# Optimization experiments

Hardware: AMD Instinct MI355X
Metric: run time of the kernel (lower is better)

## Reference

```python
import jax, jax.numpy as jnp
import numpy as np
import math

DIM = 384; HEADS = 12; HD = 32; L_REL = 4; L_STD = 12; MLP_H = 4 * DIM
B = 8; N = 256
N_REL = 1
TIME_SCALE = 30000.0 / 500 * 0.3
SCALE = HD ** -0.5
NEG = -1e9  # finite stand-in for -inf padding mask (identical softmax result, safe grads)


def _ln(x, g, b):
    m = x.mean(-1, keepdims=True)
    v = ((x - m) ** 2).mean(-1, keepdims=True)
    return (x - m) / jnp.sqrt(v + 1e-5) * g + b


def _sin_emb(x, dim):
    half = dim // 2
    freq = jnp.exp(jnp.arange(half, dtype=x.dtype) * (-math.log(10000.0) / half))
    e = x[..., None] * freq
    return jnp.concatenate([jnp.sin(e), jnp.cos(e)], -1)


def _rel_bias(x0, w1d, b1d, wp, bp):
    pos = x0[..., :3]
    t = x0[..., 3:4]
    dpos = pos[:, :, None] - pos[:, None, :]                 # [B,N,N,3]
    dt = t[:, :, None] - t[:, None, :] * TIME_SCALE          # [B,N,N,1] (scale on 2nd term, as in torch)
    dpos2 = dpos ** 2
    dt2 = dt ** 2
    ds2 = dpos2.sum(-1) - dt2[..., 0]
    d = jnp.sign(ds2) * jnp.sqrt(jnp.abs(ds2))
    f = jnp.concatenate([dpos, dt, dpos2, dt2], -1)          # [B,N,N,8]
    d = d + (f @ w1d.T + b1d)[..., 0]
    emb = _sin_emb(1024.0 * jnp.clip(d, -4.0, 4.0), HD)      # [B,N,N,HD]
    return emb @ wp.T + bp


def _mask_bias(mask):
    mn = jnp.minimum(mask[:, None, :], mask[:, :, None])
    mx = jnp.maximum(mask[:, None, :], mask[:, :, None])
    return jnp.where(mx < 0, 0.0, mn)                        # [B,N,N]


def _attn(xq, xkv, wq, wk, wv, wo, bo, rel, mbias):
    Bq, Nq, _ = xq.shape
    q = (xq @ wq.T).reshape(Bq, Nq, HEADS, HD).transpose(0, 2, 1, 3) * SCALE
    k = (xkv @ wk.T).reshape(Bq, Nq, HEADS, HD).transpose(0, 2, 1, 3)
    v = (xkv @ wv.T).reshape(Bq, Nq, HEADS, HD).transpose(0, 2, 1, 3)
    a = jnp.einsum('bhic,bhjc->bhij', q, k)
    if rel is not None:
        a = a + jnp.einsum('bhic,bijc->bhij', q, rel)
    if mbias is not None:
        a = a + mbias[:, None]
    a = jax.nn.softmax(a, axis=-1)
    o = jnp.einsum('bhij,bhjc->bihc', a, v)
    if rel is not None:
        o = o + jnp.einsum('bhij,bijc->bihc', a, rel)
    return o.reshape(Bq, Nq, HEADS * HD) @ wo.T + bo


def _mlp(x, w1, b1, w2, b2):
    return jax.nn.gelu(x @ w1.T + b1, approximate=False) @ w2.T + b2


def setup_inputs() -> dict:
    key = jax.random.key(0)
    ks = iter(jax.random.split(key, 64))
    f = lambda shape: jax.random.normal(next(ks), shape, jnp.float32) * 0.02
    inp = {}
    inp['x'] = jax.random.normal(next(ks), (B, N, DIM), jnp.float32)
    inp['x0'] = jax.random.normal(next(ks), (B, N, 4), jnp.float32)
    lengths = jax.random.randint(next(ks), (B,), N // 2, N + 1)
    inp['mask'] = jnp.where(jnp.arange(N)[None, :] < lengths[:, None], 0.0, NEG).astype(jnp.float32)
    inp['rp_w1d'] = f((1, 8)); inp['rp_b1d'] = jnp.zeros((1,), jnp.float32)
    inp['rp_wp'] = f((HD, HD)); inp['rp_bp'] = jnp.zeros((HD,), jnp.float32)
    for p, L in (('sw', L_REL), ('bl', L_STD)):
        inp[p + '_ln1_g'] = jnp.ones((L, DIM), jnp.float32); inp[p + '_ln1_b'] = jnp.zeros((L, DIM), jnp.float32)
        inp[p + '_ln2_g'] = jnp.ones((L, DIM), jnp.float32); inp[p + '_ln2_b'] = jnp.zeros((L, DIM), jnp.float32)
        inp[p + '_wq'] = f((L, DIM, DIM)); inp[p + '_wk'] = f((L, DIM, DIM)); inp[p + '_wv'] = f((L, DIM, DIM))
        inp[p + '_wo'] = f((L, DIM, DIM)); inp[p + '_bo'] = jnp.zeros((L, DIM), jnp.float32)
        inp[p + '_w1'] = f((L, MLP_H, DIM)); inp[p + '_b1'] = jnp.zeros((L, MLP_H), jnp.float32)
        inp[p + '_w2'] = f((L, DIM, MLP_H)); inp[p + '_b2'] = jnp.zeros((L, DIM), jnp.float32)
    inp['bl_g1'] = jnp.ones((L_STD, DIM), jnp.float32)   # init_values=1
    inp['bl_g2'] = jnp.ones((L_STD, DIM), jnp.float32)
    inp['cls_w'] = f((DIM,))
    inp['out_w'] = f((3, DIM)); inp['out_b'] = jnp.zeros((3,), jnp.float32)
    return inp


def reference(x, x0, mask, rp_w1d, rp_b1d, rp_wp, rp_bp,
              sw_ln1_g, sw_ln1_b, sw_ln2_g, sw_ln2_b, sw_wq, sw_wk, sw_wv, sw_wo, sw_bo,
              sw_w1, sw_b1, sw_w2, sw_b2,
              bl_ln1_g, bl_ln1_b, bl_ln2_g, bl_ln2_b, bl_wq, bl_wk, bl_wv, bl_wo, bl_bo,
              bl_w1, bl_b1, bl_w2, bl_b2, bl_g1, bl_g2, cls_w, out_w, out_b):
    rel = _rel_bias(x0, rp_w1d, rp_b1d, rp_wp, rp_bp)
    mbias = _mask_bias(mask)
    for i in range(L_REL):
        r = rel if i < N_REL else None
        xn = _ln(x, sw_ln1_g[i], sw_ln1_b[i])
        x = x + _attn(xn, xn, sw_wq[i], sw_wk[i], sw_wv[i], sw_wo[i], sw_bo[i], r, mbias)
        x = x + _mlp(_ln(x, sw_ln2_g[i], sw_ln2_b[i]), sw_w1[i], sw_b1[i], sw_w2[i], sw_b2[i])
    # prepend cls token; it is always valid
    cls = jnp.broadcast_to(cls_w[None, None, :], (x.shape[0], 1, DIM))
    x = jnp.concatenate([cls, x], axis=1)
    mask2 = jnp.concatenate([jnp.zeros((x.shape[0], 1), mask.dtype), mask], axis=1)
    mbias2 = _mask_bias(mask2)
    for i in range(L_STD):
        xn = _ln(x, bl_ln1_g[i], bl_ln1_b[i])
        x = x + bl_g1[i] * _attn(xn, xn, bl_wq[i], bl_wk[i], bl_wv[i], bl_wo[i], bl_bo[i], None, mbias2)
        x = x + bl_g2[i] * _mlp(_ln(x, bl_ln2_g[i], bl_ln2_b[i]), bl_w1[i], bl_b1[i], bl_w2[i], bl_b2[i])
    return x[:, 0] @ out_w.T + out_b   # [B, 3]
```

## Files before the change

kernel.cpp:

```cpp
#include <hip/hip_runtime.h>
#include <hip/hip_bf16.h>
#include <math.h>

#define DIM 384
#define HEADS 12
#define HD 32
#define MLP_H 1536
#define BATCH 8
#define N1 256
#define N2 257
#define QP 1152
#define SCALE 0.17677669529663687f
#define TIME_SCALE 18.0f

typedef __attribute__((ext_vector_type(8))) short frag8;
typedef __attribute__((ext_vector_type(4))) float f32x4;

__device__ inline short f2bf(float x) {
    __hip_bfloat16 h = __float2bfloat16(x);
    short s;
    __builtin_memcpy(&s, &h, 2);
    return s;
}
__device__ inline float bf2f(short s) {
    unsigned u = ((unsigned)(unsigned short)s) << 16;
    float f;
    __builtin_memcpy(&f, &u, 4);
    return f;
}

__global__ __launch_bounds__(256) void conv_kernel(
        const float* __restrict__ in, short* __restrict__ out, int n) {
    int i = (blockIdx.x * 256 + threadIdx.x) * 4;
    if (i >= n) return;
    float4 v = *(const float4*)(in + i);
    out[i]     = f2bf(v.x);
    out[i + 1] = f2bf(v.y);
    out[i + 2] = f2bf(v.z);
    out[i + 3] = f2bf(v.w);
}

__global__ __launch_bounds__(256) void conv_qkv_kernel(
        const float* __restrict__ wq, const float* __restrict__ wk,
        const float* __restrict__ wv, short* __restrict__ out, int L) {
    size_t idx = ((size_t)blockIdx.x * 256 + threadIdx.x) * 4;
    size_t total = (size_t)L * QP * DIM;
    if (idx >= total) return;
    size_t k = idx % DIM;
    size_t row = idx / DIM;
    size_t r = row % QP;
    size_t l = row / QP;
    int which = (int)(r / DIM);
    int rr = (int)(r % DIM);
    const float* src = ((which == 0) ? wq : (which == 1) ? wk : wv)
                     + (l * DIM + rr) * DIM + k;
    float4 v = *(const float4*)src;
    out[idx]     = f2bf(v.x);
    out[idx + 1] = f2bf(v.y);
    out[idx + 2] = f2bf(v.z);
    out[idx + 3] = f2bf(v.w);
}

__global__ __launch_bounds__(256) void rel_kernel(
        const float* __restrict__ x0, const float* __restrict__ w1d,
        const float* __restrict__ b1d, const float* __restrict__ wp,
        const float* __restrict__ bp, short* __restrict__ rel) {
    __shared__ float sw1[8];
    __shared__ float sb1s[1];
    __shared__ short scr[4][64][40];
    int tid = threadIdx.x;
    int w = tid >> 6, lane = tid & 63;
    int n = lane & 15, quad = lane >> 4;
    if (tid < 8) sw1[tid] = w1d[tid];
    if (tid == 0) sb1s[0] = b1d[0];

    frag8 wb0, wb1;
    #pragma unroll
    for (int e = 0; e < 8; e++) {
        wb0[e] = f2bf(wp[n * 32 + quad * 8 + e]);
        wb1[e] = f2bf(wp[(n + 16) * 32 + quad * 8 + e]);
    }
    float bp0 = bp[n], bp1 = bp[n + 16];
    __syncthreads();
    float sb1 = sb1s[0];

    int gbase = blockIdx.x * 256 + w * 64;
    int gid = gbase + lane;
    int j  = gid & (N1 - 1);
    int bi = gid >> 8;
    int i  = bi & (N1 - 1);
    int b  = bi >> 8;

    const float* pi = x0 + (size_t)(b * N1 + i) * 4;
    const float* pj = x0 + (size_t)(b * N1 + j) * 4;
    float dx = pi[0] - pj[0], dy = pi[1] - pj[1], dz = pi[2] - pj[2];
    float dt = pi[3] - pj[3] * TIME_SCALE;
    float dx2 = dx * dx, dy2 = dy * dy, dz2 = dz * dz, dt2 = dt * dt;
    float ds2 = dx2 + dy2 + dz2 - dt2;
    float d = copysignf(sqrtf(fabsf(ds2)), ds2);
    d += dx * sw1[0] + dy * sw1[1] + dz * sw1[2] + dt * sw1[3]
       + dx2 * sw1[4] + dy2 * sw1[5] + dz2 * sw1[6] + dt2 * sw1[7] + sb1;
    d = fminf(fmaxf(d, -4.f), 4.f) * 1024.f;

    const float freq[16] = {
        1.0f, 0.56234132519f, 0.31622776602f, 0.17782794100f,
        0.1f, 0.056234132519f, 0.031622776602f, 0.017782794100f,
        0.01f, 0.0056234132519f, 0.0031622776602f, 0.0017782794100f,
        0.001f, 0.00056234132519f, 0.00031622776602f, 0.00017782794100f};
    #pragma unroll
    for (int k = 0; k < 16; k++) {
        float rev = d * freq[k] * 0.15915494309189535f;
        rev = rev - floorf(rev);
        float s = __builtin_amdgcn_sinf(rev);
        float c = __builtin_amdgcn_cosf(rev);
        scr[w][lane][k]      = f2bf(s);
        scr[w][lane][16 + k] = f2bf(c);
    }

    #pragma unroll
    for (int g16 = 0; g16 < 4; g16++) {
        frag8 ea = *(const frag8*)&scr[w][g16 * 16 + n][quad * 8];
        f32x4 z = {0.f, 0.f, 0.f, 0.f};
        f32x4 s0 = __builtin_amdgcn_mfma_f32_16x16x32_bf16(ea, wb0, z, 0, 0, 0);
        f32x4 s1 = __builtin_amdgcn_mfma_f32_16x16x32_bf16(ea, wb1, z, 0, 0, 0);
        #pragma unroll
        for (int r = 0; r < 4; r++) {
            scr[w][g16 * 16 + quad * 4 + r][n]      = f2bf(s0[r] + bp0);
            scr[w][g16 * 16 + quad * 4 + r][n + 16] = f2bf(s1[r] + bp1);
        }
    }

    short* dst = rel + (size_t)gbase * HD;
    #pragma unroll
    for (int s = 0; s < 4; s++) {
        frag8 v = *(const frag8*)&scr[w][s * 16 + (lane >> 2)][(lane & 3) * 8];
        *(frag8*)(dst + s * 512 + lane * 8) = v;
    }
}

__global__ __launch_bounds__(256) void rel_score_kernel(
        const short* __restrict__ qkv, const short* __restrict__ relb,
        short* __restrict__ rs) {
    int tid = threadIdx.x;
    int w = tid >> 6, lane = tid & 63;
    int n = lane & 15, quad = lane >> 4;
    int i = blockIdx.x * 4 + w;
    int b = blockIdx.y;

    const frag8 fz = {0, 0, 0, 0, 0, 0, 0, 0};
    frag8 qa = fz;
    if (n < HEADS)
        qa = *(const frag8*)(qkv + ((size_t)(b * N1) + i) * QP + n * HD + quad * 8);

    const short* relrow = relb + (((size_t)(b * N1) + i) * N1) * HD;
    const f32x4 z = {0.f, 0.f, 0.f, 0.f};

    #pragma unroll 4
    for (int jt = 0; jt < 16; jt++) {
        frag8 rb = *(const frag8*)(relrow + (size_t)(jt * 16 + n) * HD + quad * 8);
        f32x4 s = __builtin_amdgcn_mfma_f32_16x16x32_bf16(qa, rb, z, 0, 0, 0);
        #pragma unroll
        for (int r = 0; r < 4; r++) {
            int h = quad * 4 + r;
            if (h < HEADS)
                rs[((size_t)(b * HEADS + h) * N1 + i) * N1 + jt * 16 + n] =
                    f2bf(s[r] * SCALE);
        }
    }
}

__global__ __launch_bounds__(256) void rel_pv_kernel(
        const short* __restrict__ pglob, const short* __restrict__ relb,
        const float* __restrict__ omain, short* __restrict__ ob) {
    __shared__ short vt[4][2][2][64][8];
    int tid = threadIdx.x;
    int w = tid >> 6, lane = tid & 63;
    int n = lane & 15, quad = lane >> 4;
    int i = blockIdx.x * 4 + w;
    int b = blockIdx.y;
    size_t rowB = (size_t)(b * N1);

    const frag8 fz = {0, 0, 0, 0, 0, 0, 0, 0};
    f32x4 oa0 = {0.f, 0.f, 0.f, 0.f}, oa1 = {0.f, 0.f, 0.f, 0.f};
    const short* relrow = relb + ((rowB + i) * (size_t)N1) * HD;
    const short* prow = pglob + ((size_t)(b * HEADS + (n < HEADS ? n : 0)) * N1 + i) * N1;
    bool hval = (n < HEADS);

    int jr = lane & 31;
    int cb = (lane >> 5) * 16;

    #pragma unroll 2
    for (int kk = 0; kk < 8; kk++) {
        int par = kk & 1;
        const short* rr = relrow + (size_t)(kk * 32 + jr) * HD + cb;
        frag8 rv0 = *(const frag8*)rr;
        frag8 rv1 = *(const frag8*)(rr + 8);
        #pragma unroll
        for (int e = 0; e < 8; e++) {
            int c0 = cb + e, c1 = cb + 8 + e;
            vt[w][par][c0 >> 4][(jr >> 3) * 16 + (c0 & 15)][jr & 7] = rv0[e];
            vt[w][par][c1 >> 4][(jr >> 3) * 16 + (c1 & 15)][jr & 7] = rv1[e];
        }
        frag8 pa = fz;
        if (hval) pa = *(const frag8*)(prow + kk * 32 + quad * 8);
        frag8 b0 = *(const frag8*)&vt[w][par][0][lane][0];
        frag8 b1 = *(const frag8*)&vt[w][par][1][lane][0];
        oa0 = __builtin_amdgcn_mfma_f32_16x16x32_bf16(pa, b0, oa0, 0, 0, 0);
        oa1 = __builtin_amdgcn_mfma_f32_16x16x32_bf16(pa, b1, oa1, 0, 0, 0);
    }

    #pragma unroll
    for (int r = 0; r < 4; r++) {
        int h = quad * 4 + r;
        if (h < HEADS) {
            size_t o0 = (rowB + i) * DIM + h * HD + n;
            ob[o0]      = f2bf(omain[o0]      + oa0[r]);
            ob[o0 + 16] = f2bf(omain[o0 + 16] + oa1[r]);
        }
    }
}

__global__ __launch_bounds__(128) void ln_kernel(
        const float* __restrict__ x, const float* __restrict__ g,
        const float* __restrict__ b, short* __restrict__ y) {
    int r = blockIdx.x;
    int t = threadIdx.x;
    const float* xr = x + (size_t)r * DIM;
    float v0 = xr[t], v1 = xr[t + 128], v2 = xr[t + 256];
    __shared__ float redm[2], redv[2];
    float s = v0 + v1 + v2;
    for (int o = 32; o; o >>= 1) s += __shfl_down(s, o, 64);
    int lane = t & 63, wid = t >> 6;
    if (!lane) redm[wid] = s;
    __syncthreads();
    float mean = (redm[0] + redm[1]) * (1.f / DIM);
    float d0 = v0 - mean, d1 = v1 - mean, d2 = v2 - mean;
    float s2 = d0 * d0 + d1 * d1 + d2 * d2;
    for (int o = 32; o; o >>= 1) s2 += __shfl_down(s2, o, 64);
    if (!lane) redv[wid] = s2;
    __syncthreads();
    float var = (redv[0] + redv[1]) * (1.f / DIM);
    float rs = rsqrtf(var + 1e-5f);
    short* yr = y + (size_t)r * DIM;
    yr[t]       = f2bf(d0 * rs * g[t]       + b[t]);
    yr[t + 128] = f2bf(d1 * rs * g[t + 128] + b[t + 128]);
    yr[t + 256] = f2bf(d2 * rs * g[t + 256] + b[t + 256]);
}

__global__ __launch_bounds__(512) void gemm_bf16_kernel(
        const short* __restrict__ A, const short* __restrict__ W,
        const float* __restrict__ bias, const float* __restrict__ resid,
        const float* __restrict__ gvec, float* __restrict__ Cf,
        short* __restrict__ Cb, int M, int Np, int K, int mode) {
    __shared__ short As2[2][2][4][64][8];
    __shared__ short Bs2[2][2][4][64][8];
    int tid = threadIdx.x;
    int w = tid >> 6, lane = tid & 63;
    int nlo = lane & 15, quad = lane >> 4;
    int g = w >> 2, wl = w & 3;
    int wm = wl >> 1, wn = wl & 1;
    int n0 = blockIdx.x * 64, m0 = blockIdx.y * 64;

    f32x4 acc00 = {0.f, 0.f, 0.f, 0.f}, acc01 = {0.f, 0.f, 0.f, 0.f};
    f32x4 acc10 = {0.f, 0.f, 0.f, 0.f}, acc11 = {0.f, 0.f, 0.f, 0.f};

    int oct16 = tid & 15, rbase = tid >> 4;
    int kh_s = oct16 >> 3, oo = oct16 & 7, ks_s = oo >> 2, q_s = oo & 3;
    const frag8 fz = {0, 0, 0, 0, 0, 0, 0, 0};
    frag8 pa0 = fz, pa1 = fz, pb0, pb1;

    {
        int gm0 = m0 + rbase, gm1 = m0 + rbase + 32;
        if (gm0 < M) pa0 = *(const frag8*)(A + (size_t)gm0 * K + oct16 * 8);
        if (gm1 < M) pa1 = *(const frag8*)(A + (size_t)gm1 * K + oct16 * 8);
        pb0 = *(const frag8*)(W + (size_t)(n0 + rbase) * K + oct16 * 8);
        pb1 = *(const frag8*)(W + (size_t)(n0 + rbase + 32) * K + oct16 * 8);
    }

    for (int k0 = 0; k0 < K; k0 += 128) {
        *(frag8*)&As2[kh_s][ks_s][q_s][rbase][0]      = pa0;
        *(frag8*)&As2[kh_s][ks_s][q_s][rbase + 32][0] = pa1;
        *(frag8*)&Bs2[kh_s][ks_s][q_s][rbase][0]      = pb0;
        *(frag8*)&Bs2[kh_s][ks_s][q_s][rbase + 32][0] = pb1;
        __syncthreads();
        int kn = k0 + 128;
        if (kn < K) {
            int gm0 = m0 + rbase, gm1 = m0 + rbase + 32;
            pa0 = fz; pa1 = fz;
            if (gm0 < M) pa0 = *(const frag8*)(A + (size_t)gm0 * K + kn + oct16 * 8);
            if (gm1 < M) pa1 = *(const frag8*)(A + (size_t)gm1 * K + kn + oct16 * 8);
            pb0 = *(const frag8*)(W + (size_t)(n0 + rbase) * K + kn + oct16 * 8);
            pb1 = *(const frag8*)(W + (size_t)(n0 + rbase + 32) * K + kn + oct16 * 8);
        }
        #pragma unroll
        for (int ks = 0; ks < 2; ks++) {
            frag8 a0 = *(const frag8*)&As2[g][ks][quad][wm * 32 + nlo][0];
            frag8 a1 = *(const frag8*)&As2[g][ks][quad][wm * 32 + 16 + nlo][0];
            frag8 b0 = *(const frag8*)&Bs2[g][ks][quad][wn * 32 + nlo][0];
            frag8 b1 = *(const frag8*)&Bs2[g][ks][quad][wn * 32 + 16 + nlo][0];
            acc00 = __builtin_amdgcn_mfma_f32_16x16x32_bf16(a0, b0, acc00, 0, 0, 0);
            acc01 = __builtin_amdgcn_mfma_f32_16x16x32_bf16(a0, b1, acc01, 0, 0, 0);
            acc10 = __builtin_amdgcn_mfma_f32_16x16x32_bf16(a1, b0, acc10, 0, 0, 0);
            acc11 = __builtin_amdgcn_mfma_f32_16x16x32_bf16(a1, b1, acc11, 0, 0, 0);
        }
        __syncthreads();
    }

    f32x4* red4 = (f32x4*)&As2[0][0][0][0][0];
    int roff = wl * 64 + lane;
    if (g == 1) {
        red4[roff]       = acc00;
        red4[256 + roff] = acc01;
        red4[512 + roff] = acc10;
        red4[768 + roff] = acc11;
    }
    __syncthreads();
    if (g == 1) return;
    {
        f32x4 t0 = red4[roff], t1 = red4[256 + roff];
        f32x4 t2 = red4[512 + roff], t3 = red4[768 + roff];
        #pragma unroll
        for (int r = 0; r < 4; r++) {
            acc00[r] += t0[r]; acc01[r] += t1[r];
            acc10[r] += t2[r]; acc11[r] += t3[r];
        }
    }

    #pragma unroll
    for (int mi = 0; mi < 2; mi++) {
        #pragma unroll
        for (int nf = 0; nf < 2; nf++) {
            f32x4 av = (mi == 0) ? ((nf == 0) ? acc00 : acc01)
                                 : ((nf == 0) ? acc10 : acc11);
            int col = n0 + wn * 32 + nf * 16 + nlo;
            float bcol = (mode >= 1) ? bias[col] : 0.f;
            float gs = 1.f;
            if (mode == 2 && gvec) gs = gvec[col];
            #pragma unroll
            for (int r = 0; r < 4; r++) {
                int row = m0 + wm * 32 + mi * 16 + quad * 4 + r;
                if (row >= M) continue;
                float v = av[r] + bcol;
                if (mode == 1) v = 0.5f * v * (1.f + erff(v * 0.70710678118654752f));
                if (mode == 2) {
                    Cf[(size_t)row * Np + col] = resid[(size_t)row * Np + col] + gs * v;
                } else {
                    Cb[(size_t)row * Np + col] = f2bf(v);
                }
            }
        }
    }
}

__global__ __launch_bounds__(256) void attn_mfma_kernel(
        const short* __restrict__ qkv, const float* __restrict__ maskv,
        short* __restrict__ ob, int Nseq) {
    __shared__ short kf[18][64][8];
    __shared__ short vf[9][2][64][8];
    __shared__ short pbuf[4][2][16][40];
    __shared__ float ms[320];

    int tid = threadIdx.x;
    int w = tid >> 6, lane = tid & 63;
    int n = lane & 15, quad = lane >> 4;
    int qg = blockIdx.x, h = blockIdx.y, b = blockIdx.z;
    size_t rowB = (size_t)(b * Nseq);

    for (int j = tid; j < 320; j += 256)
        ms[j] = (j < Nseq) ? maskv[b * Nseq + j] : 0.f;

    {
        int c0 = (tid & 3) * 8;
        for (int j = tid >> 2; j < 288; j += 64) {
            frag8 kk = {0, 0, 0, 0, 0, 0, 0, 0};
            frag8 vv = {0, 0, 0, 0, 0, 0, 0, 0};
            if (j < Nseq) {
                const short* base = qkv + (rowB + j) * QP + h * HD + c0;
                kk = *(const frag8*)(base + 384);
                vv = *(const frag8*)(base + 768);
            }
            *(frag8*)&kf[j >> 4][(c0 >> 3) * 16 + (j & 15)][0] = kk;
            #pragma unroll
            for (int e = 0; e < 8; e++) {
                int c = c0 + e;
                vf[j >> 5][c >> 4][((j & 31) >> 3) * 16 + (c & 15)][j & 7] = vv[e];
            }
        }
    }

    int i0 = qg * 64 + w * 16;
    frag8 qa = {0, 0, 0, 0, 0, 0, 0, 0};
    {
        int i = i0 + n;
        if (i < Nseq) qa = *(const frag8*)(qkv + (rowB + i) * QP + h * HD + quad * 8);
    }
    __syncthreads();

    float msq[4];
    #pragma unroll
    for (int r = 0; r < 4; r++) msq[r] = ms[i0 + quad * 4 + r];

    float mrow[4], lsum[4];
    #pragma unroll
    for (int r = 0; r < 4; r++) { mrow[r] = -3.0e38f; lsum[r] = 0.f; }
    f32x4 oacc0 = {0.f, 0.f, 0.f, 0.f}, oacc1 = {0.f, 0.f, 0.f, 0.f};

    for (int jb = 0; jb < 9; jb++) {
        int par = jb & 1;
        frag8 kb0 = *(const frag8*)&kf[2 * jb][lane][0];
        frag8 kb1 = *(const frag8*)&kf[2 * jb + 1][lane][0];
        f32x4 z = {0.f, 0.f, 0.f, 0.f};
        f32x4 s0 = __builtin_amdgcn_mfma_f32_16x16x32_bf16(qa, kb0, z, 0, 0, 0);
        f32x4 s1 = __builtin_amdgcn_mfma_f32_16x16x32_bf16(qa, kb1, z, 0, 0, 0);

        int j0 = jb * 32 + n;
        int j1 = j0 + 16;
        float mj0 = ms[j0], mj1 = ms[j1];
        float pad0 = (j0 < Nseq) ? 0.f : -1e9f;
        float pad1 = (j1 < Nseq) ? 0.f : -1e9f;

        #pragma unroll
        for (int r = 0; r < 4; r++) {
            float mi = msq[r];
            float b0 = ((fmaxf(mi, mj0) < 0.f) ? 0.f : fminf(mi, mj0)) + pad0;
            float b1 = ((fmaxf(mi, mj1) < 0.f) ? 0.f : fminf(mi, mj1)) + pad1;
            float v0 = s0[r] * SCALE + b0;
            float v1 = s1[r] * SCALE + b1;
            float rm = fmaxf(v0, v1);
            rm = fmaxf(rm, __shfl_xor(rm, 1));
            rm = fmaxf(rm, __shfl_xor(rm, 2));
            rm = fmaxf(rm, __shfl_xor(rm, 4));
            rm = fmaxf(rm, __shfl_xor(rm, 8));
            float mn = fmaxf(mrow[r], rm);
            float alpha = __expf(mrow[r] - mn);
            mrow[r] = mn;
            float p0 = __expf(v0 - mn);
            float p1 = __expf(v1 - mn);
            float ps = p0 + p1;
            ps += __shfl_xor(ps, 1);
            ps += __shfl_xor(ps, 2);
            ps += __shfl_xor(ps, 4);
            ps += __shfl_xor(ps, 8);
            lsum[r] = lsum[r] * alpha + ps;
            oacc0[r] *= alpha;
            oacc1[r] *= alpha;
            pbuf[w][par][quad * 4 + r][n]      = f2bf(p0);
            pbuf[w][par][quad * 4 + r][n + 16] = f2bf(p1);
        }
        frag8 pa = *(const frag8*)&pbuf[w][par][n][quad * 8];
        frag8 vb0 = *(const frag8*)&vf[jb][0][lane][0];
        frag8 vb1 = *(const frag8*)&vf[jb][1][lane][0];
        oacc0 = __builtin_amdgcn_mfma_f32_16x16x32_bf16(pa, vb0, oacc0, 0, 0, 0);
        oacc1 = __builtin_amdgcn_mfma_f32_16x16x32_bf16(pa, vb1, oacc1, 0, 0, 0);
    }

    #pragma unroll
    for (int r = 0; r < 4; r++) {
        int i = i0 + quad * 4 + r;
        if (i < Nseq) {
            float invl = 1.f / lsum[r];
            ob[(rowB + i) * DIM + h * HD + n]      = f2bf(oacc0[r] * invl);
            ob[(rowB + i) * DIM + h * HD + 16 + n] = f2bf(oacc1[r] * invl);
        }
    }
}

__global__ __launch_bounds__(128) void attn_rel_mfma_kernel(
        const short* __restrict__ qkv, short* __restrict__ rs,
        const float* __restrict__ maskv, float* __restrict__ omain) {
    const int Nseq = N1;
    __shared__ short kf[16][64][8];
    __shared__ short vf[8][2][64][8];
    __shared__ short pbuf[2][2][16][40];
    __shared__ float ms[256];

    int tid = threadIdx.x;
    int w = tid >> 6, lane = tid & 63;
    int n = lane & 15, quad = lane >> 4;
    int qg = blockIdx.x, h = blockIdx.y, b = blockIdx.z;
    size_t rowB = (size_t)(b * Nseq);

    for (int jj = tid; jj < 256; jj += 128) ms[jj] = maskv[b * Nseq + jj];

    {
        int c0 = (tid & 3) * 8;
        for (int j = tid >> 2; j < 256; j += 32) {
            const short* base = qkv + (rowB + j) * QP + h * HD + c0;
            frag8 kk = *(const frag8*)(base + 384);
            frag8 vv = *(const frag8*)(base + 768);
            *(frag8*)&kf[j >> 4][(c0 >> 3) * 16 + (j & 15)][0] = kk;
            #pragma unroll
            for (int e = 0; e < 8; e++) {
                int c = c0 + e;
                vf[j >> 5][c >> 4][((j & 31) >> 3) * 16 + (c & 15)][j & 7] = vv[e];
            }
        }
    }

    int i0 = qg * 32 + w * 16;
    frag8 qa = *(const frag8*)(qkv + (rowB + i0 + n) * QP + h * HD + quad * 8);
    __syncthreads();

    float msq[4];
    short* rsp[4];
    #pragma unroll
    for (int r = 0; r < 4; r++) {
        msq[r] = ms[i0 + quad * 4 + r];
        rsp[r] = rs + ((size_t)(b * HEADS + h) * N1 + (i0 + quad * 4 + r)) * N1;
    }

    float sv0[32], sv1[32];
    float rmax[4];
    #pragma unroll
    for (int r = 0; r < 4; r++) rmax[r] = -3.0e38f;

    #pragma unroll
    for (int jb = 0; jb < 8; jb++) {
        frag8 kb0 = *(const frag8*)&kf[2 * jb][lane][0];
        frag8 kb1 = *(const frag8*)&kf[2 * jb + 1][lane][0];
        f32x4 z = {0.f, 0.f, 0.f, 0.f};
        f32x4 s0 = __builtin_amdgcn_mfma_f32_16x16x32_bf16(qa, kb0, z, 0, 0, 0);
        f32x4 s1 = __builtin_amdgcn_mfma_f32_16x16x32_bf16(qa, kb1, z, 0, 0, 0);
        int j0 = jb * 32 + n;
        int j1 = j0 + 16;
        float mj0 = ms[j0], mj1 = ms[j1];
        #pragma unroll
        for (int r = 0; r < 4; r++) {
            float d0 = bf2f(rsp[r][j0]);
            float d1 = bf2f(rsp[r][j1]);
            float mi = msq[r];
            float b0 = (fmaxf(mi, mj0) < 0.f) ? 0.f : fminf(mi, mj0);
            float b1 = (fmaxf(mi, mj1) < 0.f) ? 0.f : fminf(mi, mj1);
            float v0 = s0[r] * SCALE + d0 + b0;
            float v1 = s1[r] * SCALE + d1 + b1;
            sv0[jb * 4 + r] = v0;
            sv1[jb * 4 + r] = v1;
            rmax[r] = fmaxf(rmax[r], fmaxf(v0, v1));
        }
    }
    #pragma unroll
    for (int r = 0; r < 4; r++) {
        float rm = rmax[r];
        rm = fmaxf(rm, __shfl_xor(rm, 1));
        rm = fmaxf(rm, __shfl_xor(rm, 2));
        rm = fmaxf(rm, __shfl_xor(rm, 4));
        rm = fmaxf(rm, __shfl_xor(rm, 8));
        rmax[r] = rm;
    }

    float lsum[4] = {0.f, 0.f, 0.f, 0.f};
    #pragma unroll
    for (int jb = 0; jb < 8; jb++) {
        #pragma unroll
        for (int r = 0; r < 4; r++) {
            float p0 = __expf(sv0[jb * 4 + r] - rmax[r]);
            float p1 = __expf(sv1[jb * 4 + r] - rmax[r]);
            sv0[jb * 4 + r] = p0;
            sv1[jb * 4 + r] = p1;
            lsum[r] += p0 + p1;
        }
    }
    float invl[4];
    #pragma unroll
    for (int r = 0; r < 4; r++) {
        float ls = lsum[r];
        ls += __shfl_xor(ls, 1);
        ls += __shfl_xor(ls, 2);
        ls += __shfl_xor(ls, 4);
        ls += __shfl_xor(ls, 8);
        invl[r] = 1.f / ls;
    }

    f32x4 oacc0 = {0.f, 0.f, 0.f, 0.f}, oacc1 = {0.f, 0.f, 0.f, 0.f};
    #pragma unroll
    for (int jb = 0; jb < 8; jb++) {
        int par = jb & 1;
        #pragma unroll
        for (int r = 0; r < 4; r++) {
            short h0 = f2bf(sv0[jb * 4 + r] * invl[r]);
            short h1 = f2bf(sv1[jb * 4 + r] * invl[r]);
            pbuf[w][par][quad * 4 + r][n]      = h0;
            pbuf[w][par][quad * 4 + r][n + 16] = h1;
            rsp[r][jb * 32 + n]      = h0;
            rsp[r][jb * 32 + n + 16] = h1;
        }
        frag8 pa = *(const frag8*)&pbuf[w][par][n][quad * 8];
        frag8 vb0 = *(const frag8*)&vf[jb][0][lane][0];
        frag8 vb1 = *(const frag8*)&vf[jb][1][lane][0];
        oacc0 = __builtin_amdgcn_mfma_f32_16x16x32_bf16(pa, vb0, oacc0, 0, 0, 0);
        oacc1 = __builtin_amdgcn_mfma_f32_16x16x32_bf16(pa, vb1, oacc1, 0, 0, 0);
    }

    #pragma unroll
    for (int r = 0; r < 4; r++) {
        int i = i0 + quad * 4 + r;
        omain[(rowB + i) * DIM + h * HD + n]      = oacc0[r];
        omain[(rowB + i) * DIM + h * HD + 16 + n] = oacc1[r];
    }
}

__global__ __launch_bounds__(256) void concat_kernel(
        const float* __restrict__ xa, const float* __restrict__ clsw,
        const float* __restrict__ mask, float* __restrict__ xb,
        float* __restrict__ m2) {
    int idx = blockIdx.x * 256 + threadIdx.x;
    const int total = BATCH * N2 * DIM;
    if (idx < total) {
        int c = idx % DIM;
        int tokb = idx / DIM;
        int p = tokb % N2, b = tokb / N2;
        xb[idx] = (p == 0) ? clsw[c] : xa[((size_t)(b * N1) + p - 1) * DIM + c];
    }
    if (idx < BATCH * N2) {
        int p = idx % N2, b = idx / N2;
        m2[idx] = (p == 0) ? 0.f : mask[b * N1 + p - 1];
    }
}

__global__ __launch_bounds__(64) void head_kernel(
        const float* __restrict__ xb, const float* __restrict__ ow,
        const float* __restrict__ obv, float* __restrict__ out) {
    int blk = blockIdx.x;
    int b = blk / 3, o = blk % 3;
    int lane = threadIdx.x;
    const float* xr = xb + (size_t)(b * N2) * DIM;
    const float* wr = ow + o * DIM;
    float s = 0.f;
    for (int c = lane; c < DIM; c += 64) s += xr[c] * wr[c];
    for (int off = 32; off; off >>= 1) s += __shfl_down(s, off, 64);
    if (!lane) out[blk] = s + obv[o];
}

extern "C" void kernel_launch(void* const* d_in, const int* in_sizes, int n_in,
                              void* d_out, int out_size, void* d_ws, size_t ws_size,
                              hipStream_t stream) {
    (void)in_sizes; (void)n_in; (void)out_size; (void)ws_size;
    const float* X       = (const float*)d_in[0];
    const float* X0      = (const float*)d_in[1];
    const float* MSK     = (const float*)d_in[2];
    const float* RW1     = (const float*)d_in[3];
    const float* RB1     = (const float*)d_in[4];
    const float* RWP     = (const float*)d_in[5];
    const float* RBP     = (const float*)d_in[6];
    const float* SW_LN1G = (const float*)d_in[7];
    const float* SW_LN1B = (const float*)d_in[8];
    const float* SW_LN2G = (const float*)d_in[9];
    const float* SW_LN2B = (const float*)d_in[10];
    const float* SW_WQ   = (const float*)d_in[11];
    const float* SW_WK   = (const float*)d_in[12];
    const float* SW_WV   = (const float*)d_in[13];
    const float* SW_WO   = (const float*)d_in[14];
    const float* SW_BO   = (const float*)d_in[15];
    const float* SW_W1   = (const float*)d_in[16];
    const float* SW_B1   = (const float*)d_in[17];
    const float* SW_W2   = (const float*)d_in[18];
    const float* SW_B2   = (const float*)d_in[19];
    const float* BL_LN1G = (const float*)d_in[20];
    const float* BL_LN1B = (const float*)d_in[21];
    const float* BL_LN2G = (const float*)d_in[22];
    const float* BL_LN2B = (const float*)d_in[23];
    const float* BL_WQ   = (const float*)d_in[24];
    const float* BL_WK   = (const float*)d_in[25];
    const float* BL_WV   = (const float*)d_in[26];
    const float* BL_WO   = (const float*)d_in[27];
    const float* BL_BO   = (const float*)d_in[28];
    const float* BL_W1   = (const float*)d_in[29];
    const float* BL_B1   = (const float*)d_in[30];
    const float* BL_W2   = (const float*)d_in[31];
    const float* BL_B2   = (const float*)d_in[32];
    const float* BL_G1   = (const float*)d_in[33];
    const float* BL_G2   = (const float*)d_in[34];
    const float* CLSW    = (const float*)d_in[35];
    const float* OUTW    = (const float*)d_in[36];
    const float* OUTB    = (const float*)d_in[37];

    const int T1 = BATCH * N1;
    const int T2 = BATCH * N2;
    const size_t RELSZ = (size_t)BATCH * N1 * N1 * HD;

    short* rel = (short*)d_ws;
    float* xa  = (float*)(rel + RELSZ);
    float* xb  = xa + (size_t)T1 * DIM;
    float* m2  = xb + (size_t)T2 * DIM;
    short* sbase = (short*)(m2 + 2064);
    short* xn   = sbase;
    short* qkv  = xn  + (size_t)T2 * DIM;
    short* ab   = qkv + (size_t)T2 * QP;
    short* hb   = ab  + (size_t)T2 * DIM;
    short* cw_qkv_sw = hb + (size_t)T2 * MLP_H;
    short* cw_qkv_bl = cw_qkv_sw + (size_t)4  * QP * DIM;
    short* cw_wo_sw  = cw_qkv_bl + (size_t)12 * QP * DIM;
    short* cw_wo_bl  = cw_wo_sw  + (size_t)4  * DIM * DIM;
    short* cw_w1_sw  = cw_wo_bl  + (size_t)12 * DIM * DIM;
    short* cw_w1_bl  = cw_w1_sw  + (size_t)4  * MLP_H * DIM;
    short* cw_w2_sw  = cw_w1_bl  + (size_t)12 * MLP_H * DIM;
    short* cw_w2_bl  = cw_w2_sw  + (size_t)4  * DIM * MLP_H;
    short* rs_buf    = cw_w2_bl  + (size_t)12 * DIM * MLP_H;
    float* omain     = (float*)hb;

    conv_qkv_kernel<<<(4 * QP * DIM / 4 + 255) / 256, 256, 0, stream>>>(SW_WQ, SW_WK, SW_WV, cw_qkv_sw, 4);
    conv_qkv_kernel<<<(12 * QP * DIM / 4 + 255) / 256, 256, 0, stream>>>(BL_WQ, BL_WK, BL_WV, cw_qkv_bl, 12);
    conv_kernel<<<(4 * DIM * DIM / 4 + 255) / 256, 256, 0, stream>>>(SW_WO, cw_wo_sw, 4 * DIM * DIM);
    conv_kernel<<<(12 * DIM * DIM / 4 + 255) / 256, 256, 0, stream>>>(BL_WO, cw_wo_bl, 12 * DIM * DIM);
    conv_kernel<<<(4 * MLP_H * DIM / 4 + 255) / 256, 256, 0, stream>>>(SW_W1, cw_w1_sw, 4 * MLP_H * DIM);
    conv_kernel<<<(12 * MLP_H * DIM / 4 + 255) / 256, 256, 0, stream>>>(BL_W1, cw_w1_bl, 12 * MLP_H * DIM);
    conv_kernel<<<(4 * DIM * MLP_H / 4 + 255) / 256, 256, 0, stream>>>(SW_W2, cw_w2_sw, 4 * DIM * MLP_H);
    conv_kernel<<<(12 * DIM * MLP_H / 4 + 255) / 256, 256, 0, stream>>>(BL_W2, cw_w2_bl, 12 * DIM * MLP_H);

    rel_kernel<<<BATCH * N1 * N1 / 256, 256, 0, stream>>>(X0, RW1, RB1, RWP, RBP, rel);
    hipMemcpyAsync(xa, X, sizeof(float) * T1 * DIM, hipMemcpyDeviceToDevice, stream);

    dim3 gQ1(QP / 64, T1 / 64);
    dim3 gP1(DIM / 64, T1 / 64);
    dim3 gM1(MLP_H / 64, T1 / 64);
    dim3 gF1(4, HEADS, BATCH);
    dim3 gRel(8, HEADS, BATCH);
    for (int l = 0; l < 4; l++) {
        const short* wqkv = cw_qkv_sw + (size_t)l * QP * DIM;
        const short* wo = cw_wo_sw + (size_t)l * DIM * DIM;
        const short* w1 = cw_w1_sw + (size_t)l * MLP_H * DIM;
        const short* w2 = cw_w2_sw + (size_t)l * DIM * MLP_H;
        const float* bo = SW_BO + (size_t)l * DIM;
        const float* b1 = SW_B1 + (size_t)l * MLP_H;
        const float* b2 = SW_B2 + (size_t)l * DIM;

        ln_kernel<<<T1, 128, 0, stream>>>(xa, SW_LN1G + l * DIM, SW_LN1B + l * DIM, xn);
        gemm_bf16_kernel<<<gQ1, 512, 0, stream>>>(xn, wqkv, nullptr, nullptr, nullptr,
                                                  nullptr, qkv, T1, QP, DIM, 0);
        if (l == 0) {
            rel_score_kernel<<<dim3(N1 / 4, BATCH), 256, 0, stream>>>(qkv, rel, rs_buf);
            attn_rel_mfma_kernel<<<gRel, 128, 0, stream>>>(qkv, rs_buf, MSK, omain);
            rel_pv_kernel<<<dim3(N1 / 4, BATCH), 256, 0, stream>>>(rs_buf, rel, omain, ab);
        } else {
            attn_mfma_kernel<<<gF1, 256, 0, stream>>>(qkv, MSK, ab, N1);
        }
        gemm_bf16_kernel<<<gP1, 512, 0, stream>>>(ab, wo, bo, xa, nullptr,
                                                  xa, nullptr, T1, DIM, DIM, 2);
        ln_kernel<<<T1, 128, 0, stream>>>(xa, SW_LN2G + l * DIM, SW_LN2B + l * DIM, xn);
        gemm_bf16_kernel<<<gM1, 512, 0, stream>>>(xn, w1, b1, nullptr, nullptr,
                                                  nullptr, hb, T1, MLP_H, DIM, 1);
        gemm_bf16_kernel<<<gP1, 512, 0, stream>>>(hb, w2, b2, xa, nullptr,
                                                  xa, nullptr, T1, DIM, MLP_H, 2);
    }

    concat_kernel<<<(BATCH * N2 * DIM + 255) / 256, 256, 0, stream>>>(xa, CLSW, MSK, xb, m2);

    int MB2 = (T2 + 63) / 64;
    dim3 gQ2(QP / 64, MB2);
    dim3 gP2(DIM / 64, MB2);
    dim3 gM2(MLP_H / 64, MB2);
    dim3 gF2(5, HEADS, BATCH);
    for (int l = 0; l < 12; l++) {
        const short* wqkv = cw_qkv_bl + (size_t)l * QP * DIM;
        const short* wo = cw_wo_bl + (size_t)l * DIM * DIM;
        const short* w1 = cw_w1_bl + (size_t)l * MLP_H * DIM;
        const short* w2 = cw_w2_bl + (size_t)l * DIM * MLP_H;
        const float* bo = BL_BO + (size_t)l * DIM;
        const float* b1 = BL_B1 + (size_t)l * MLP_H;
        const float* b2 = BL_B2 + (size_t)l * DIM;
        const float* g1 = BL_G1 + (size_t)l * DIM;
        const float* g2 = BL_G2 + (size_t)l * DIM;

        ln_kernel<<<T2, 128, 0, stream>>>(xb, BL_LN1G + l * DIM, BL_LN1B + l * DIM, xn);
        gemm_bf16_kernel<<<gQ2, 512, 0, stream>>>(xn, wqkv, nullptr, nullptr, nullptr,
                                                  nullptr, qkv, T2, QP, DIM, 0);
        attn_mfma_kernel<<<gF2, 256, 0, stream>>>(qkv, m2, ab, N2);
        gemm_bf16_kernel<<<gP2, 512, 0, stream>>>(ab, wo, bo, xb, g1,
                                                  xb, nullptr, T2, DIM, DIM, 2);
        ln_kernel<<<T2, 128, 0, stream>>>(xb, BL_LN2G + l * DIM, BL_LN2B + l * DIM, xn);
        gemm_bf16_kernel<<<gM2, 512, 0, stream>>>(xn, w1, b1, nullptr, nullptr,
                                                  nullptr, hb, T2, MLP_H, DIM, 1);
        gemm_bf16_kernel<<<gP2, 512, 0, stream>>>(hb, w2, b2, xb, g2,
                                                  xb, nullptr, T2, DIM, MLP_H, 2);
    }

    head_kernel<<<BATCH * 3, 64, 0, stream>>>(xb, OUTW, OUTB, (float*)d_out);
}
```

Baseline: 1.728 ms.

## Split-K the output and MLP-down GEMMs with atomic residual accumulation; merge weight conversions

The N=384 projection GEMMs (attention output and MLP down) are now split along K into 3 or 4 slices across blockIdx.z. Each slice atomically adds its partial product into the fp32 residual stream, and only slice 0 adds the bias. This is meant to raise the block count for these narrow GEMMs, which otherwise launch only 6x32 blocks. Separately, six weight-conversion launches are merged into one kernel to cut launch overhead. The cost is float atomics on the residual buffer, which make the summation order non-deterministic, and extra reads and writes of the output.

```diff
diff --git a/kernel.cpp b/kernel.cpp
--- a/kernel.cpp
+++ b/kernel.cpp
@@ -29,10 +29,24 @@
     return f;
 }
 
-__global__ __launch_bounds__(256) void conv_kernel(
-        const float* __restrict__ in, short* __restrict__ out, int n) {
-    int i = (blockIdx.x * 256 + threadIdx.x) * 4;
-    if (i >= n) return;
+__global__ __launch_bounds__(256) void conv6_kernel(
+        const float* __restrict__ p0, short* __restrict__ q0, int n0,
+        const float* __restrict__ p1, short* __restrict__ q1, int n1,
+        const float* __restrict__ p2, short* __restrict__ q2, int n2,
+        const float* __restrict__ p3, short* __restrict__ q3, int n3,
+        const float* __restrict__ p4, short* __restrict__ q4, int n4,
+        const float* __restrict__ p5, short* __restrict__ q5, int n5) {
+    (void)n5;
+    int blk = blockIdx.x;
+    int b0 = n0 >> 10, b1 = n1 >> 10, b2 = n2 >> 10, b3 = n3 >> 10, b4 = n4 >> 10;
+    const float* in; short* out;
+    if (blk < b0)              { in = p0; out = q0; }
+    else if ((blk -= b0) < b1) { in = p1; out = q1; }
+    else if ((blk -= b1) < b2) { in = p2; out = q2; }
+    else if ((blk -= b2) < b3) { in = p3; out = q3; }
+    else if ((blk -= b3) < b4) { in = p4; out = q4; }
+    else { blk -= b4;            in = p5; out = q5; }
+    int i = blk * 1024 + threadIdx.x * 4;
     float4 v = *(const float4*)(in + i);
     out[i]     = f2bf(v.x);
     out[i + 1] = f2bf(v.y);
@@ -249,9 +263,9 @@
 
 __global__ __launch_bounds__(512) void gemm_bf16_kernel(
         const short* __restrict__ A, const short* __restrict__ W,
-        const float* __restrict__ bias, const float* __restrict__ resid,
-        const float* __restrict__ gvec, float* __restrict__ Cf,
-        short* __restrict__ Cb, int M, int Np, int K, int mode) {
+        const float* __restrict__ bias, const float* __restrict__ gvec,
+        float* __restrict__ Cf, short* __restrict__ Cb,
+        int M, int Np, int K, int mode, int Kz) {
     __shared__ short As2[2][2][4][64][8];
     __shared__ short Bs2[2][2][4][64][8];
     int tid = threadIdx.x;
@@ -260,6 +274,9 @@
     int g = w >> 2, wl = w & 3;
     int wm = wl >> 1, wn = wl & 1;
     int n0 = blockIdx.x * 64, m0 = blockIdx.y * 64;
+    int kbeg = blockIdx.z * Kz;
+    int kend = kbeg + Kz;
+    if (kend > K) kend = K;
 
     f32x4 acc00 = {0.f, 0.f, 0.f, 0.f}, acc01 = {0.f, 0.f, 0.f, 0.f};
     f32x4 acc10 = {0.f, 0.f, 0.f, 0.f}, acc11 = {0.f, 0.f, 0.f, 0.f};
@@ -271,20 +288,20 @@
 
     {
         int gm0 = m0 + rbase, gm1 = m0 + rbase + 32;
-        if (gm0 < M) pa0 = *(const frag8*)(A + (size_t)gm0 * K + oct16 * 8);
-        if (gm1 < M) pa1 = *(const frag8*)(A + (size_t)gm1 * K + oct16 * 8);
-        pb0 = *(const frag8*)(W + (size_t)(n0 + rbase) * K + oct16 * 8);
-        pb1 = *(const frag8*)(W + (size_t)(n0 + rbase + 32) * K + oct16 * 8);
-    }
-
-    for (int k0 = 0; k0 < K; k0 += 128) {
+        if (gm0 < M) pa0 = *(const frag8*)(A + (size_t)gm0 * K + kbeg + oct16 * 8);
+        if (gm1 < M) pa1 = *(const frag8*)(A + (size_t)gm1 * K + kbeg + oct16 * 8);
+        pb0 = *(const frag8*)(W + (size_t)(n0 + rbase) * K + kbeg + oct16 * 8);
+        pb1 = *(const frag8*)(W + (size_t)(n0 + rbase + 32) * K + kbeg + oct16 * 8);
+    }
+
+    for (int k0 = kbeg; k0 < kend; k0 += 128) {
         *(frag8*)&As2[kh_s][ks_s][q_s][rbase][0]      = pa0;
         *(frag8*)&As2[kh_s][ks_s][q_s][rbase + 32][0] = pa1;
         *(frag8*)&Bs2[kh_s][ks_s][q_s][rbase][0]      = pb0;
         *(frag8*)&Bs2[kh_s][ks_s][q_s][rbase + 32][0] = pb1;
         __syncthreads();
         int kn = k0 + 128;
-        if (kn < K) {
+        if (kn < kend) {
             int gm0 = m0 + rbase, gm1 = m0 + rbase + 32;
             pa0 = fz; pa1 = fz;
             if (gm0 < M) pa0 = *(const frag8*)(A + (size_t)gm0 * K + kn + oct16 * 8);
@@ -333,7 +350,8 @@
             f32x4 av = (mi == 0) ? ((nf == 0) ? acc00 : acc01)
                                  : ((nf == 0) ? acc10 : acc11);
             int col = n0 + wn * 32 + nf * 16 + nlo;
-            float bcol = (mode >= 1) ? bias[col] : 0.f;
+            float bcol = 0.f;
+            if (mode == 1 || (mode == 2 && blockIdx.z == 0)) bcol = bias[col];
             float gs = 1.f;
             if (mode == 2 && gvec) gs = gvec[col];
             #pragma unroll
@@ -343,7 +361,7 @@
                 float v = av[r] + bcol;
                 if (mode == 1) v = 0.5f * v * (1.f + erff(v * 0.70710678118654752f));
                 if (mode == 2) {
-                    Cf[(size_t)row * Np + col] = resid[(size_t)row * Np + col] + gs * v;
+                    atomicAdd(&Cf[(size_t)row * Np + col], gs * v);
                 } else {
                     Cb[(size_t)row * Np + col] = f2bf(v);
                 }
@@ -700,19 +718,24 @@
 
     conv_qkv_kernel<<<(4 * QP * DIM / 4 + 255) / 256, 256, 0, stream>>>(SW_WQ, SW_WK, SW_WV, cw_qkv_sw, 4);
     conv_qkv_kernel<<<(12 * QP * DIM / 4 + 255) / 256, 256, 0, stream>>>(BL_WQ, BL_WK, BL_WV, cw_qkv_bl, 12);
-    conv_kernel<<<(4 * DIM * DIM / 4 + 255) / 256, 256, 0, stream>>>(SW_WO, cw_wo_sw, 4 * DIM * DIM);
-    conv_kernel<<<(12 * DIM * DIM / 4 + 255) / 256, 256, 0, stream>>>(BL_WO, cw_wo_bl, 12 * DIM * DIM);
-    conv_kernel<<<(4 * MLP_H * DIM / 4 + 255) / 256, 256, 0, stream>>>(SW_W1, cw_w1_sw, 4 * MLP_H * DIM);
-    conv_kernel<<<(12 * MLP_H * DIM / 4 + 255) / 256, 256, 0, stream>>>(BL_W1, cw_w1_bl, 12 * MLP_H * DIM);
-    conv_kernel<<<(4 * DIM * MLP_H / 4 + 255) / 256, 256, 0, stream>>>(SW_W2, cw_w2_sw, 4 * DIM * MLP_H);
-    conv_kernel<<<(12 * DIM * MLP_H / 4 + 255) / 256, 256, 0, stream>>>(BL_W2, cw_w2_bl, 12 * DIM * MLP_H);
+    {
+        int e0 = 4 * DIM * DIM, e1 = 12 * DIM * DIM;
+        int e2 = 4 * MLP_H * DIM, e3 = 12 * MLP_H * DIM;
+        int e4 = 4 * DIM * MLP_H, e5 = 12 * DIM * MLP_H;
+        int nblk = (e0 + e1 + e2 + e3 + e4 + e5) >> 10;
+        conv6_kernel<<<nblk, 256, 0, stream>>>(
+            SW_WO, cw_wo_sw, e0, BL_WO, cw_wo_bl, e1,
+            SW_W1, cw_w1_sw, e2, BL_W1, cw_w1_bl, e3,
+            SW_W2, cw_w2_sw, e4, BL_W2, cw_w2_bl, e5);
+    }
 
     rel_kernel<<<BATCH * N1 * N1 / 256, 256, 0, stream>>>(X0, RW1, RB1, RWP, RBP, rel);
     hipMemcpyAsync(xa, X, sizeof(float) * T1 * DIM, hipMemcpyDeviceToDevice, stream);
 
     dim3 gQ1(QP / 64, T1 / 64);
-    dim3 gP1(DIM / 64, T1 / 64);
+    dim3 gP1z(DIM / 64, T1 / 64, 3);
     dim3 gM1(MLP_H / 64, T1 / 64);
+    dim3 gW1z(DIM / 64, T1 / 64, 4);
     dim3 gF1(4, HEADS, BATCH);
     dim3 gRel(8, HEADS, BATCH);
     for (int l = 0; l < 4; l++) {
@@ -725,8 +748,8 @@
         const float* b2 = SW_B2 + (size_t)l * DIM;
 
         ln_kernel<<<T1, 128, 0, stream>>>(xa, SW_LN1G + l * DIM, SW_LN1B + l * DIM, xn);
-        gemm_bf16_kernel<<<gQ1, 512, 0, stream>>>(xn, wqkv, nullptr, nullptr, nullptr,
-                                                  nullptr, qkv, T1, QP, DIM, 0);
+        gemm_bf16_kernel<<<gQ1, 512, 0, stream>>>(xn, wqkv, nullptr, nullptr,
+                                                  nullptr, qkv, T1, QP, DIM, 0, DIM);
         if (l == 0) {
             rel_score_kernel<<<dim3(N1 / 4, BATCH), 256, 0, stream>>>(qkv, rel, rs_buf);
             attn_rel_mfma_kernel<<<gRel, 128, 0, stream>>>(qkv, rs_buf, MSK, omain);
@@ -734,21 +757,22 @@
         } else {
             attn_mfma_kernel<<<gF1, 256, 0, stream>>>(qkv, MSK, ab, N1);
         }
-        gemm_bf16_kernel<<<gP1, 512, 0, stream>>>(ab, wo, bo, xa, nullptr,
-                                                  xa, nullptr, T1, DIM, DIM, 2);
+        gemm_bf16_kernel<<<gP1z, 512, 0, stream>>>(ab, wo, bo, nullptr,
+                                                   xa, nullptr, T1, DIM, DIM, 2, 128);
         ln_kernel<<<T1, 128, 0, stream>>>(xa, SW_LN2G + l * DIM, SW_LN2B + l * DIM, xn);
-        gemm_bf16_kernel<<<gM1, 512, 0, stream>>>(xn, w1, b1, nullptr, nullptr,
-                                                  nullptr, hb, T1, MLP_H, DIM, 1);
-        gemm_bf16_kernel<<<gP1, 512, 0, stream>>>(hb, w2, b2, xa, nullptr,
-                                                  xa, nullptr, T1, DIM, MLP_H, 2);
+        gemm_bf16_kernel<<<gM1, 512, 0, stream>>>(xn, w1, b1, nullptr,
+                                                  nullptr, hb, T1, MLP_H, DIM, 1, DIM);
+        gemm_bf16_kernel<<<gW1z, 512, 0, stream>>>(hb, w2, b2, nullptr,
+                                                   xa, nullptr, T1, DIM, MLP_H, 2, 384);
     }
 
     concat_kernel<<<(BATCH * N2 * DIM + 255) / 256, 256, 0, stream>>>(xa, CLSW, MSK, xb, m2);
 
     int MB2 = (T2 + 63) / 64;
     dim3 gQ2(QP / 64, MB2);
-    dim3 gP2(DIM / 64, MB2);
+    dim3 gP2z(DIM / 64, MB2, 3);
     dim3 gM2(MLP_H / 64, MB2);
+    dim3 gW2z(DIM / 64, MB2, 4);
     dim3 gF2(5, HEADS, BATCH);
     for (int l = 0; l < 12; l++) {
         const short* wqkv = cw_qkv_bl + (size_t)l * QP * DIM;
@@ -762,16 +786,16 @@
         const float* g2 = BL_G2 + (size_t)l * DIM;
 
         ln_kernel<<<T2, 128, 0, stream>>>(xb, BL_LN1G + l * DIM, BL_LN1B + l * DIM, xn);
-        gemm_bf16_kernel<<<gQ2, 512, 0, stream>>>(xn, wqkv, nullptr, nullptr, nullptr,
-                                                  nullptr, qkv, T2, QP, DIM, 0);
+        gemm_bf16_kernel<<<gQ2, 512, 0, stream>>>(xn, wqkv, nullptr, nullptr,
+                                                  nullptr, qkv, T2, QP, DIM, 0, DIM);
         attn_mfma_kernel<<<gF2, 256, 0, stream>>>(qkv, m2, ab, N2);
-        gemm_bf16_kernel<<<gP2, 512, 0, stream>>>(ab, wo, bo, xb, g1,
-                                                  xb, nullptr, T2, DIM, DIM, 2);
+        gemm_bf16_kernel<<<gP2z, 512, 0, stream>>>(ab, wo, bo, g1,
+                                                   xb, nullptr, T2, DIM, DIM, 2, 128);
         ln_kernel<<<T2, 128, 0, stream>>>(xb, BL_LN2G + l * DIM, BL_LN2B + l * DIM, xn);
-        gemm_bf16_kernel<<<gM2, 512, 0, stream>>>(xn, w1, b1, nullptr, nullptr,
-                                                  nullptr, hb, T2, MLP_H, DIM, 1);
-        gemm_bf16_kernel<<<gP2, 512, 0, stream>>>(hb, w2, b2, xb, g2,
-                                                  xb, nullptr, T2, DIM, MLP_H, 2);
+        gemm_bf16_kernel<<<gM2, 512, 0, stream>>>(xn, w1, b1, nullptr,
+                                                  nullptr, hb, T2, MLP_H, DIM, 1, DIM);
+        gemm_bf16_kernel<<<gW2z, 512, 0, stream>>>(hb, w2, b2, g2,
+                                                   xb, nullptr, T2, DIM, MLP_H, 2, 384);
     }
 
     head_kernel<<<BATCH * 3, 64, 0, stream>>>(xb, OUTW, OUTB, (float*)d_out);
```

Result: no change. 1.725 ms (-0.2%).
